# Kernel optimization log

Measured on AMD Instinct MI355X. Metric: run time of the kernel, lower is better.

The kernel has to match this reference:

```python
import jax, jax.numpy as jnp
import numpy as np

N = 100000
NNZ = 3200000
K = 3

def setup_inputs() -> dict:
    key = jax.random.key(0)
    ks = jax.random.split(key, 9)
    return {
        "x": jax.random.normal(ks[0], (N, 128), dtype=jnp.float32),
        "vals": jax.random.uniform(ks[1], (NNZ,), dtype=jnp.float32) * (1.0 / 32.0),
        "W1": jax.random.normal(ks[2], (128 * K, 256), dtype=jnp.float32) * 0.05,
        "b1": jax.random.normal(ks[3], (256,), dtype=jnp.float32) * 0.05,
        "W2": jax.random.normal(ks[4], (256 * K, 64), dtype=jnp.float32) * 0.05,
        "b2": jax.random.normal(ks[5], (64,), dtype=jnp.float32) * 0.05,
        "rows": jax.random.randint(ks[6], (NNZ,), 0, N, dtype=jnp.int32),
        "cols": jax.random.randint(ks[7], (NNZ,), 0, N, dtype=jnp.int32),
        "idx": jax.random.randint(ks[8], (50000,), 0, N, dtype=jnp.int32),
    }

def _spmm(rows, cols, vals, x):
    # sparse [N,N] @ dense [N,F] via gather + segment_sum
    return jax.ops.segment_sum(vals[:, None] * x[cols], rows, num_segments=N)

def _cheb_basis(x, rows, cols, vals, k):
    # Chebyshev recurrence: T0=x, T1=L x, T_m = 2 L T_{m-1} - T_{m-2}
    xs = [x]
    if k > 1:
        x0, x1 = x, _spmm(rows, cols, vals, x)
        xs.append(x1)
        for _ in range(2, k):
            x2 = 2.0 * _spmm(rows, cols, vals, x1) - x0
            xs.append(x2)
            x0, x1 = x1, x2
    # match torch layout: [N, F, K] -> [N, F*K] (per-feature K contiguous)
    return jnp.stack(xs, axis=2).reshape(x.shape[0], -1)

def reference(x, vals, W1, b1, W2, b2, rows, cols, idx):
    h = _cheb_basis(x, rows, cols, vals, K) @ W1 + b1
    h = jax.nn.relu(h)  # dropout omitted (eval mode)
    out = _cheb_basis(h, rows, cols, vals, K) @ W2 + b2
    return out[idx]
```

## Files before the change

kernel.cpp:

```cpp
#include <hip/hip_runtime.h>
#include <hip/hip_bf16.h>

typedef __attribute__((ext_vector_type(8))) __bf16 bf16x8;
typedef __attribute__((ext_vector_type(4))) float floatx4;
typedef unsigned short ushort_t;
typedef unsigned int uint_t;

#define N_NODES 100000
#define NNZ_E   3200000
#define N_IDX   50000
#define NB_BKT  196
#define PTILE   8192
#define PBLOCKS 391

__device__ __forceinline__ float bf2f(uint_t u16) {
  union { float f; uint_t i; } v; v.i = u16 << 16; return v.f;
}
__device__ __forceinline__ unsigned short f2bf(float f) {
  union { float f; uint_t i; } v; v.f = f;
  uint_t x = v.i;
  return (unsigned short)((x + 0x7FFFu + ((x >> 16) & 1u)) >> 16);
}


__global__ __launch_bounds__(256) void k_bhist(const int* __restrict__ rows,
                                               int* __restrict__ bcnt) {
  __shared__ int h[NB_BKT];
  for (int i = threadIdx.x; i < NB_BKT; i += 256) h[i] = 0;
  __syncthreads();
  int base = blockIdx.x * PTILE;
  for (int i = threadIdx.x; i < PTILE; i += 256) {
    int e = base + i;
    if (e < NNZ_E) atomicAdd(&h[rows[e] >> 9], 1);
  }
  __syncthreads();
  for (int i = threadIdx.x; i < NB_BKT; i += 256)
    if (h[i]) atomicAdd(&bcnt[i], h[i]);
}

__global__ void k_bscan(const int* __restrict__ bcnt, int* __restrict__ bbase,
                        int* __restrict__ bcur) {
  __shared__ int ts[256];
  int t = threadIdx.x;
  int v = (t < NB_BKT) ? bcnt[t] : 0;
  ts[t] = v;
  __syncthreads();
  for (int off = 1; off < 256; off <<= 1) {
    int x = ts[t];
    int a = (t >= off) ? ts[t - off] : 0;
    __syncthreads();
    ts[t] = x + a;
    __syncthreads();
  }
  if (t < NB_BKT) {
    int b = (t == 0) ? 0 : ts[t - 1];
    bbase[t] = b;
    bcur[t] = b;
  }
}

__global__ __launch_bounds__(256) void k_part(const int* __restrict__ rows,
                                              const int* __restrict__ cols,
                                              const float* __restrict__ vals,
                                              int* __restrict__ bcur,
                                              int2* __restrict__ tmp) {
  __shared__ int h[NB_BKT];
  for (int i = threadIdx.x; i < NB_BKT; i += 256) h[i] = 0;
  __syncthreads();
  int base = blockIdx.x * PTILE;
  for (int i = threadIdx.x; i < PTILE; i += 256) {
    int e = base + i;
    if (e < NNZ_E) atomicAdd(&h[rows[e] >> 9], 1);
  }
  __syncthreads();
  for (int i = threadIdx.x; i < NB_BKT; i += 256) {
    int c = h[i];
    h[i] = c ? atomicAdd(&bcur[i], c) : 0;
  }
  __syncthreads();
  for (int i = threadIdx.x; i < PTILE; i += 256) {
    int e = base + i;
    if (e < NNZ_E) {
      int rr = rows[e];
      int p = atomicAdd(&h[rr >> 9], 1);
      int2 o;
      o.x = cols[e] | ((rr & 511) << 17);
      o.y = __float_as_int(vals[e]);
      tmp[p] = o;
    }
  }
}

__global__ __launch_bounds__(512) void k_sort(const int* __restrict__ bbase,
                                              const int2* __restrict__ tmp,
                                              int2* __restrict__ edges,
                                              int* __restrict__ rowptr) {
  __shared__ int cnt[512];
  __shared__ int ts[512];
  int b = blockIdx.x, t = threadIdx.x;
  int s = bbase[b];
  int epos = (b == NB_BKT - 1) ? NNZ_E : bbase[b + 1];
  cnt[t] = 0;
  __syncthreads();
  for (int i = s + t; i < epos; i += 512)
    atomicAdd(&cnt[(tmp[i].x >> 17) & 511], 1);
  __syncthreads();
  ts[t] = cnt[t];
  __syncthreads();
  for (int off = 1; off < 512; off <<= 1) {
    int x = ts[t];
    int a = (t >= off) ? ts[t - off] : 0;
    __syncthreads();
    ts[t] = x + a;
    __syncthreads();
  }
  int pre = (t == 0) ? 0 : ts[t - 1];
  int grow = b * 512 + t;
  if (grow < N_NODES) rowptr[grow] = s + pre;
  cnt[t] = s + pre;
  __syncthreads();
  for (int i = s + t; i < epos; i += 512) {
    int2 p = tmp[i];
    int rl = (p.x >> 17) & 511;
    int pos = atomicAdd(&cnt[rl], 1);
    int2 o;
    o.x = p.x & 0x1FFFF;
    o.y = p.y;
    edges[pos] = o;
  }
  if (b == 0 && t == 0) rowptr[N_NODES] = NNZ_E;
}


__global__ void k_cvt(const float4* __restrict__ x, ushort4* __restrict__ xb) {
  int i = blockIdx.x * blockDim.x + threadIdx.x;
  if (i < N_NODES * 128 / 4) {
    float4 v = x[i];
    ushort4 o;
    o.x = f2bf(v.x); o.y = f2bf(v.y); o.z = f2bf(v.z); o.w = f2bf(v.w);
    xb[i] = o;
  }
}


__global__ void k_prepW1(const float* __restrict__ W, ushort_t* __restrict__ Wp) {
  int kp = blockIdx.x;
  int n  = threadIdx.x;
  int ch = kp >> 7;
  int f  = kp & 127;
  float v;
  if (ch == 0)      v = W[(f*3+0)*256+n] - W[(f*3+2)*256+n];
  else if (ch == 1) v = W[(f*3+1)*256+n];
  else              v = 2.0f * W[(f*3+2)*256+n];
  int kb = kp >> 5, kr = kp & 31;
  int lane = ((kr >> 3) << 4) | (n & 15);
  Wp[(((size_t)kb * 16 + (n >> 4)) * 64 + lane) * 8 + (kr & 7)] = f2bf(v);
}

__global__ void k_prepW2(const float* __restrict__ W, ushort_t* __restrict__ Wp) {
  int f = blockIdx.x;
  int c = threadIdx.x;
  int g = c >> 6, n = c & 63;
  float v;
  if (g == 0)      v = W[(f*3+0)*64+n] - W[(f*3+2)*64+n];
  else if (g == 1) v = W[(f*3+1)*64+n];
  else             v = 2.0f * W[(f*3+2)*64+n];
  int kb = f >> 5, kr = f & 31;
  int nb = c >> 4;
  int lane = ((kr >> 3) << 4) | (c & 15);
  Wp[(((size_t)kb * 12 + nb) * 64 + lane) * 8 + (kr & 7)] = f2bf(v);
}


__global__ __launch_bounds__(256) void k_spmm128(
    const int* __restrict__ rowptr, const int2* __restrict__ edges,
    const ushort_t* __restrict__ in, ushort_t* __restrict__ out) {
  int r = blockIdx.x * 4 + (threadIdx.x >> 6);
  int f = threadIdx.x & 63;
  int e0 = rowptr[r], e1 = rowptr[r + 1];
  float a0 = 0.f, a1 = 0.f;
  int e = e0;
  for (; e + 8 <= e1; e += 8) {
    int2 E[8];
#pragma unroll
    for (int j = 0; j < 8; ++j) E[j] = edges[e + j];
    uint_t q[8];
#pragma unroll
    for (int j = 0; j < 8; ++j)
      q[j] = *(const uint_t*)(in + (size_t)E[j].x * 128 + 2 * f);
#pragma unroll
    for (int j = 0; j < 8; ++j) {
      float v = __int_as_float(E[j].y);
      a0 = fmaf(v, bf2f(q[j] & 0xFFFFu), a0);
      a1 = fmaf(v, bf2f(q[j] >> 16), a1);
    }
  }
  for (; e + 4 <= e1; e += 4) {
    int2 E[4];
#pragma unroll
    for (int j = 0; j < 4; ++j) E[j] = edges[e + j];
#pragma unroll
    for (int j = 0; j < 4; ++j) {
      uint_t q = *(const uint_t*)(in + (size_t)E[j].x * 128 + 2 * f);
      float v = __int_as_float(E[j].y);
      a0 = fmaf(v, bf2f(q & 0xFFFFu), a0);
      a1 = fmaf(v, bf2f(q >> 16), a1);
    }
  }
  for (; e < e1; ++e) {
    int2 E = edges[e];
    uint_t q = *(const uint_t*)(in + (size_t)E.x * 128 + 2 * f);
    float v = __int_as_float(E.y);
    a0 = fmaf(v, bf2f(q & 0xFFFFu), a0);
    a1 = fmaf(v, bf2f(q >> 16), a1);
  }
  uint_t o = ((uint_t)f2bf(a1) << 16) | (uint_t)f2bf(a0);
  *(uint_t*)(out + (size_t)r * 128 + 2 * f) = o;
}


__global__ __launch_bounds__(256) void k_spmm64_add(
    const int* __restrict__ rowptr, const int2* __restrict__ edges,
    const ushort_t* __restrict__ p2, const ushort_t* __restrict__ p1,
    ushort_t* __restrict__ u) {
  int r = blockIdx.x * 4 + (threadIdx.x >> 6);
  int lane = threadIdx.x & 63;
  int half = lane >> 5, f = lane & 31;
  int e0 = rowptr[r], e1 = rowptr[r + 1];
  int ne = e1 - e0;
  int hs = (ne + 1) >> 1;
  int e = e0 + half * hs;
  int send = half ? e1 : (e0 + hs);
  float a0 = 0.f, a1 = 0.f;
  for (; e + 4 <= send; e += 4) {
    int2 E[4];
#pragma unroll
    for (int j = 0; j < 4; ++j) E[j] = edges[e + j];
#pragma unroll
    for (int j = 0; j < 4; ++j) {
      uint_t q = *(const uint_t*)(p2 + (size_t)E[j].x * 64 + 2 * f);
      float v = __int_as_float(E[j].y);
      a0 = fmaf(v, bf2f(q & 0xFFFFu), a0);
      a1 = fmaf(v, bf2f(q >> 16), a1);
    }
  }
  for (; e < send; ++e) {
    int2 E = edges[e];
    uint_t q = *(const uint_t*)(p2 + (size_t)E.x * 64 + 2 * f);
    float v = __int_as_float(E.y);
    a0 = fmaf(v, bf2f(q & 0xFFFFu), a0);
    a1 = fmaf(v, bf2f(q >> 16), a1);
  }
  a0 += __shfl_xor(a0, 32);
  a1 += __shfl_xor(a1, 32);
  if (half == 0) {
    uint_t pp = *(const uint_t*)(p1 + (size_t)r * 64 + 2 * f);
    float b0 = a0 + bf2f(pp & 0xFFFFu);
    float b1 = a1 + bf2f(pp >> 16);
    uint_t o = ((uint_t)f2bf(b1) << 16) | (uint_t)f2bf(b0);
    *(uint_t*)(u + (size_t)r * 64 + 2 * f) = o;
  }
}


__global__ __launch_bounds__(256) void k_spmm64_idx(
    const int* __restrict__ rowptr, const int2* __restrict__ edges,
    const ushort_t* __restrict__ u, const float* __restrict__ p0,
    const int* __restrict__ idx, float* __restrict__ out) {
  int o = blockIdx.x * 4 + (threadIdx.x >> 6);
  int r = idx[o];
  int lane = threadIdx.x & 63;
  int half = lane >> 5, f = lane & 31;
  int e0 = rowptr[r], e1 = rowptr[r + 1];
  int ne = e1 - e0;
  int hs = (ne + 1) >> 1;
  int e = e0 + half * hs;
  int send = half ? e1 : (e0 + hs);
  float a0 = 0.f, a1 = 0.f;
  for (; e + 4 <= send; e += 4) {
    int2 E[4];
#pragma unroll
    for (int j = 0; j < 4; ++j) E[j] = edges[e + j];
#pragma unroll
    for (int j = 0; j < 4; ++j) {
      uint_t q = *(const uint_t*)(u + (size_t)E[j].x * 64 + 2 * f);
      float v = __int_as_float(E[j].y);
      a0 = fmaf(v, bf2f(q & 0xFFFFu), a0);
      a1 = fmaf(v, bf2f(q >> 16), a1);
    }
  }
  for (; e < send; ++e) {
    int2 E = edges[e];
    uint_t q = *(const uint_t*)(u + (size_t)E.x * 64 + 2 * f);
    float v = __int_as_float(E.y);
    a0 = fmaf(v, bf2f(q & 0xFFFFu), a0);
    a1 = fmaf(v, bf2f(q >> 16), a1);
  }
  a0 += __shfl_xor(a0, 32);
  a1 += __shfl_xor(a1, 32);
  if (half == 0) {
    float2 b = *(const float2*)(p0 + (size_t)r * 64 + 2 * f);
    float2 w; w.x = b.x + a0; w.y = b.y + a1;
    *(float2*)(out + (size_t)o * 64 + 2 * f) = w;
  }
}


__global__ __launch_bounds__(256) void k_gemm1(
    const ushort_t* __restrict__ A0, const ushort_t* __restrict__ A1,
    const ushort_t* __restrict__ A2, const ushort_t* __restrict__ Bp,
    const float* __restrict__ bias, ushort_t* __restrict__ h) {
  int wid = (blockIdx.x * 256 + threadIdx.x) >> 6;
  int lane = threadIdx.x & 63;
  int mt = wid >> 1, ng = wid & 1;
  int mr = mt * 16 + (lane & 15);
  int ko = (lane >> 4) << 3;
  floatx4 acc[8] = {};
#pragma unroll
  for (int c = 0; c < 3; ++c) {
    const ushort_t* Ab = (c == 0 ? A0 : c == 1 ? A1 : A2) + (size_t)mr * 128 + ko;
#pragma unroll
    for (int kb = 0; kb < 4; ++kb) {
      bf16x8 a = *(const bf16x8*)(Ab + kb * 32);
      int kbg = c * 4 + kb;
      const ushort_t* Bb = Bp + (((size_t)(kbg * 16 + ng * 8)) * 64 + lane) * 8;
#pragma unroll
      for (int nt = 0; nt < 8; ++nt) {
        bf16x8 b = *(const bf16x8*)(Bb + (size_t)nt * 64 * 8);
        acc[nt] = __builtin_amdgcn_mfma_f32_16x16x32_bf16(a, b, acc[nt], 0, 0, 0);
      }
    }
  }
  int col0 = ng * 128 + (lane & 15);
  int r0 = mt * 16 + ((lane >> 4) << 2);
#pragma unroll
  for (int nt = 0; nt < 8; ++nt) {
    int col = col0 + nt * 16;
    float bv = bias[col];
#pragma unroll
    for (int rg = 0; rg < 4; ++rg) {
      float v = acc[nt][rg] + bv;
      v = v > 0.f ? v : 0.f;
      h[(size_t)(r0 + rg) * 256 + col] = f2bf(v);
    }
  }
}


__global__ __launch_bounds__(256) void k_gemm2(
    const ushort_t* __restrict__ A, const ushort_t* __restrict__ Bp,
    const float* __restrict__ bias, float* __restrict__ p0,
    ushort_t* __restrict__ p1, ushort_t* __restrict__ p2) {
  int wid = (blockIdx.x * 256 + threadIdx.x) >> 6;
  if (wid >= 18750) return;
  int lane = threadIdx.x & 63;
  int mt = wid / 3, ng = wid - mt * 3;
  int mr = mt * 16 + (lane & 15);
  int ko = (lane >> 4) << 3;
  floatx4 acc[4] = {};
  const ushort_t* Ab = A + (size_t)mr * 256 + ko;
#pragma unroll
  for (int kb = 0; kb < 8; ++kb) {
    bf16x8 a = *(const bf16x8*)(Ab + kb * 32);
    const ushort_t* Bb = Bp + (((size_t)(kb * 12 + ng * 4)) * 64 + lane) * 8;
#pragma unroll
    for (int nt = 0; nt < 4; ++nt) {
      bf16x8 b = *(const bf16x8*)(Bb + (size_t)nt * 64 * 8);
      acc[nt] = __builtin_amdgcn_mfma_f32_16x16x32_bf16(a, b, acc[nt], 0, 0, 0);
    }
  }
  int c16 = lane & 15;
  int r0 = mt * 16 + ((lane >> 4) << 2);
  if (ng == 0) {
#pragma unroll
    for (int nt = 0; nt < 4; ++nt) {
      float bv = bias[nt * 16 + c16];
#pragma unroll
      for (int rg = 0; rg < 4; ++rg)
        p0[(size_t)(r0 + rg) * 64 + nt * 16 + c16] = acc[nt][rg] + bv;
    }
  } else {
    ushort_t* dst = (ng == 1) ? p1 : p2;
#pragma unroll
    for (int nt = 0; nt < 4; ++nt)
#pragma unroll
      for (int rg = 0; rg < 4; ++rg)
        dst[(size_t)(r0 + rg) * 64 + nt * 16 + c16] = f2bf(acc[nt][rg]);
  }
}


extern "C" void kernel_launch(void* const* d_in, const int* in_sizes, int n_in,
                              void* d_out, int out_size, void* d_ws, size_t ws_size,
                              hipStream_t stream) {
  const float* x    = (const float*)d_in[0];
  const float* vals = (const float*)d_in[1];
  const float* W1   = (const float*)d_in[2];
  const float* b1   = (const float*)d_in[3];
  const float* W2   = (const float*)d_in[4];
  const float* b2   = (const float*)d_in[5];
  const int*   rows = (const int*)d_in[6];
  const int*   cols = (const int*)d_in[7];
  const int*   idx  = (const int*)d_in[8];
  float* out = (float*)d_out;

  char* w = (char*)d_ws;
  size_t off = 0;
  auto take = [&](size_t b) -> char* {
    char* p = w + off;
    off += (b + 255) & ~(size_t)255;
    return p;
  };
  int*      bcnt    = (int*)take((size_t)NB_BKT * 4);
  int*      bbase   = (int*)take((size_t)NB_BKT * 4);
  int*      bcur    = (int*)take((size_t)NB_BKT * 4);
  int*      rowptr  = (int*)take((size_t)(N_NODES + 1) * 4);
  int2*     tmp     = (int2*)take((size_t)NNZ_E * 8);
  int2*     edges   = (int2*)take((size_t)NNZ_E * 8);
  ushort_t* xb      = (ushort_t*)take((size_t)N_NODES * 128 * 2);
  ushort_t* T1a     = (ushort_t*)take((size_t)N_NODES * 128 * 2);
  ushort_t* U1      = (ushort_t*)take((size_t)N_NODES * 128 * 2);
  ushort_t* h       = (ushort_t*)take((size_t)N_NODES * 256 * 2);
  ushort_t* W1p     = (ushort_t*)take((size_t)384 * 256 * 2);
  ushort_t* W2p     = (ushort_t*)take((size_t)256 * 192 * 2);

  float*    p0 = (float*)xb;
  ushort_t* p1 = T1a;
  ushort_t* p2 = T1a + (size_t)N_NODES * 64;
  ushort_t* u  = U1;

  hipMemsetAsync(bcnt, 0, (size_t)NB_BKT * 4, stream);
  k_bhist<<<PBLOCKS, 256, 0, stream>>>(rows, bcnt);
  k_bscan<<<1, 256, 0, stream>>>(bcnt, bbase, bcur);
  k_part<<<PBLOCKS, 256, 0, stream>>>(rows, cols, vals, bcur, tmp);
  k_sort<<<NB_BKT, 512, 0, stream>>>(bbase, tmp, edges, rowptr);

  k_cvt<<<(N_NODES * 128 / 4 + 255) / 256, 256, 0, stream>>>((const float4*)x, (ushort4*)xb);
  k_prepW1<<<384, 256, 0, stream>>>(W1, W1p);
  k_prepW2<<<256, 192, 0, stream>>>(W2, W2p);

  k_spmm128<<<N_NODES / 4, 256, 0, stream>>>(rowptr, edges, xb, T1a);
  k_spmm128<<<N_NODES / 4, 256, 0, stream>>>(rowptr, edges, T1a, U1);
  k_gemm1<<<3125, 256, 0, stream>>>(xb, T1a, U1, W1p, b1, h);

  k_gemm2<<<4688, 256, 0, stream>>>(h, W2p, b2, p0, p1, p2);
  k_spmm64_add<<<N_NODES / 4, 256, 0, stream>>>(rowptr, edges, p2, p1, u);
  k_spmm64_idx<<<N_IDX / 4, 256, 0, stream>>>(rowptr, edges, u, p0, idx, out);
}
```

Baseline: 684.9 us.

## Interleave edges across half-waves with wider gathers and uniform row indices in SpMM

The SpMM kernels now split each row's edges between the two half-waves by interleaving even and odd edges, and reduce the partial sums with a cross-half shuffle. The 128-feature kernel gathers 8 bytes per lane so that each half-wave covers a full row. Row indices are forced into scalar registers with readfirstlane, and a 32-edge unrolled main loop keeps more gathers in flight. This is meant to raise memory-level parallelism and cut per-edge overhead, at the cost of higher register pressure from the 32-entry edge arrays and an extra shuffle reduction.

After: 1.238 ms. 80.8% more time.

```diff
diff --git a/kernel.cpp b/kernel.cpp
--- a/kernel.cpp
+++ b/kernel.cpp
@@ -175,47 +175,80 @@
 __global__ __launch_bounds__(256) void k_spmm128(
     const int* __restrict__ rowptr, const int2* __restrict__ edges,
     const ushort_t* __restrict__ in, ushort_t* __restrict__ out) {
-  int r = blockIdx.x * 4 + (threadIdx.x >> 6);
-  int f = threadIdx.x & 63;
+  int r = __builtin_amdgcn_readfirstlane(blockIdx.x * 4 + (threadIdx.x >> 6));
+  int lane = threadIdx.x & 63;
+  int half = lane >> 5;
+  int l5 = lane & 31;
   int e0 = rowptr[r], e1 = rowptr[r + 1];
-  float a0 = 0.f, a1 = 0.f;
+  float a0 = 0.f, a1 = 0.f, a2 = 0.f, a3 = 0.f;
   int e = e0;
+  for (; e + 32 <= e1; e += 32) {
+    int2 E[32];
+#pragma unroll
+    for (int j = 0; j < 32; ++j) E[j] = edges[e + j];
+    uint2 q[16];
+#pragma unroll
+    for (int j = 0; j < 16; ++j) {
+      int c = half ? E[2*j+1].x : E[2*j].x;
+      q[j] = *(const uint2*)(in + (size_t)c * 128 + 4 * l5);
+    }
+#pragma unroll
+    for (int j = 0; j < 16; ++j) {
+      float v = __int_as_float(half ? E[2*j+1].y : E[2*j].y);
+      a0 = fmaf(v, bf2f(q[j].x & 0xFFFFu), a0);
+      a1 = fmaf(v, bf2f(q[j].x >> 16), a1);
+      a2 = fmaf(v, bf2f(q[j].y & 0xFFFFu), a2);
+      a3 = fmaf(v, bf2f(q[j].y >> 16), a3);
+    }
+  }
   for (; e + 8 <= e1; e += 8) {
     int2 E[8];
 #pragma unroll
     for (int j = 0; j < 8; ++j) E[j] = edges[e + j];
-    uint_t q[8];
-#pragma unroll
-    for (int j = 0; j < 8; ++j)
-      q[j] = *(const uint_t*)(in + (size_t)E[j].x * 128 + 2 * f);
-#pragma unroll
-    for (int j = 0; j < 8; ++j) {
-      float v = __int_as_float(E[j].y);
-      a0 = fmaf(v, bf2f(q[j] & 0xFFFFu), a0);
-      a1 = fmaf(v, bf2f(q[j] >> 16), a1);
-    }
-  }
-  for (; e + 4 <= e1; e += 4) {
-    int2 E[4];
-#pragma unroll
-    for (int j = 0; j < 4; ++j) E[j] = edges[e + j];
+    uint2 q[4];
 #pragma unroll
     for (int j = 0; j < 4; ++j) {
-      uint_t q = *(const uint_t*)(in + (size_t)E[j].x * 128 + 2 * f);
-      float v = __int_as_float(E[j].y);
-      a0 = fmaf(v, bf2f(q & 0xFFFFu), a0);
-      a1 = fmaf(v, bf2f(q >> 16), a1);
-    }
-  }
-  for (; e < e1; ++e) {
+      int c = half ? E[2*j+1].x : E[2*j].x;
+      q[j] = *(const uint2*)(in + (size_t)c * 128 + 4 * l5);
+    }
+#pragma unroll
+    for (int j = 0; j < 4; ++j) {
+      float v = __int_as_float(half ? E[2*j+1].y : E[2*j].y);
+      a0 = fmaf(v, bf2f(q[j].x & 0xFFFFu), a0);
+      a1 = fmaf(v, bf2f(q[j].x >> 16), a1);
+      a2 = fmaf(v, bf2f(q[j].y & 0xFFFFu), a2);
+      a3 = fmaf(v, bf2f(q[j].y >> 16), a3);
+    }
+  }
+  for (; e + 2 <= e1; e += 2) {
+    int2 Ea = edges[e], Eb = edges[e + 1];
+    int c = half ? Eb.x : Ea.x;
+    uint2 q = *(const uint2*)(in + (size_t)c * 128 + 4 * l5);
+    float v = __int_as_float(half ? Eb.y : Ea.y);
+    a0 = fmaf(v, bf2f(q.x & 0xFFFFu), a0);
+    a1 = fmaf(v, bf2f(q.x >> 16), a1);
+    a2 = fmaf(v, bf2f(q.y & 0xFFFFu), a2);
+    a3 = fmaf(v, bf2f(q.y >> 16), a3);
+  }
+  if (e < e1) {
     int2 E = edges[e];
-    uint_t q = *(const uint_t*)(in + (size_t)E.x * 128 + 2 * f);
-    float v = __int_as_float(E.y);
-    a0 = fmaf(v, bf2f(q & 0xFFFFu), a0);
-    a1 = fmaf(v, bf2f(q >> 16), a1);
-  }
-  uint_t o = ((uint_t)f2bf(a1) << 16) | (uint_t)f2bf(a0);
-  *(uint_t*)(out + (size_t)r * 128 + 2 * f) = o;
+    uint2 q = *(const uint2*)(in + (size_t)E.x * 128 + 4 * l5);
+    float v = half ? 0.f : __int_as_float(E.y);
+    a0 = fmaf(v, bf2f(q.x & 0xFFFFu), a0);
+    a1 = fmaf(v, bf2f(q.x >> 16), a1);
+    a2 = fmaf(v, bf2f(q.y & 0xFFFFu), a2);
+    a3 = fmaf(v, bf2f(q.y >> 16), a3);
+  }
+  a0 += __shfl_xor(a0, 32);
+  a1 += __shfl_xor(a1, 32);
+  a2 += __shfl_xor(a2, 32);
+  a3 += __shfl_xor(a3, 32);
+  if (half == 0) {
+    uint2 o2;
+    o2.x = ((uint_t)f2bf(a1) << 16) | (uint_t)f2bf(a0);
+    o2.y = ((uint_t)f2bf(a3) << 16) | (uint_t)f2bf(a2);
+    *(uint2*)(out + (size_t)r * 128 + 4 * l5) = o2;
+  }
 }
 
 
@@ -223,42 +256,70 @@
     const int* __restrict__ rowptr, const int2* __restrict__ edges,
     const ushort_t* __restrict__ p2, const ushort_t* __restrict__ p1,
     ushort_t* __restrict__ u) {
-  int r = blockIdx.x * 4 + (threadIdx.x >> 6);
+  int r = __builtin_amdgcn_readfirstlane(blockIdx.x * 4 + (threadIdx.x >> 6));
   int lane = threadIdx.x & 63;
-  int half = lane >> 5, f = lane & 31;
+  int half = lane >> 5;
+  int l5 = lane & 31;
   int e0 = rowptr[r], e1 = rowptr[r + 1];
-  int ne = e1 - e0;
-  int hs = (ne + 1) >> 1;
-  int e = e0 + half * hs;
-  int send = half ? e1 : (e0 + hs);
   float a0 = 0.f, a1 = 0.f;
-  for (; e + 4 <= send; e += 4) {
-    int2 E[4];
-#pragma unroll
-    for (int j = 0; j < 4; ++j) E[j] = edges[e + j];
+  int e = e0;
+  for (; e + 32 <= e1; e += 32) {
+    int2 E[32];
+#pragma unroll
+    for (int j = 0; j < 32; ++j) E[j] = edges[e + j];
+    uint_t q[16];
+#pragma unroll
+    for (int j = 0; j < 16; ++j) {
+      int c = half ? E[2*j+1].x : E[2*j].x;
+      q[j] = *(const uint_t*)(p2 + (size_t)c * 64 + 2 * l5);
+    }
+#pragma unroll
+    for (int j = 0; j < 16; ++j) {
+      float v = __int_as_float(half ? E[2*j+1].y : E[2*j].y);
+      a0 = fmaf(v, bf2f(q[j] & 0xFFFFu), a0);
+      a1 = fmaf(v, bf2f(q[j] >> 16), a1);
+    }
+  }
+  for (; e + 8 <= e1; e += 8) {
+    int2 E[8];
+#pragma unroll
+    for (int j = 0; j < 8; ++j) E[j] = edges[e + j];
+    uint_t q[4];
 #pragma unroll
     for (int j = 0; j < 4; ++j) {
-      uint_t q = *(const uint_t*)(p2 + (size_t)E[j].x * 64 + 2 * f);
-      float v = __int_as_float(E[j].y);
-      a0 = fmaf(v, bf2f(q & 0xFFFFu), a0);
-      a1 = fmaf(v, bf2f(q >> 16), a1);
-    }
-  }
-  for (; e < send; ++e) {
+      int c = half ? E[2*j+1].x : E[2*j].x;
+      q[j] = *(const uint_t*)(p2 + (size_t)c * 64 + 2 * l5);
+    }
+#pragma unroll
+    for (int j = 0; j < 4; ++j) {
+      float v = __int_as_float(half ? E[2*j+1].y : E[2*j].y);
+      a0 = fmaf(v, bf2f(q[j] & 0xFFFFu), a0);
+      a1 = fmaf(v, bf2f(q[j] >> 16), a1);
+    }
+  }
+  for (; e + 2 <= e1; e += 2) {
+    int2 Ea = edges[e], Eb = edges[e + 1];
+    int c = half ? Eb.x : Ea.x;
+    uint_t q = *(const uint_t*)(p2 + (size_t)c * 64 + 2 * l5);
+    float v = __int_as_float(half ? Eb.y : Ea.y);
+    a0 = fmaf(v, bf2f(q & 0xFFFFu), a0);
+    a1 = fmaf(v, bf2f(q >> 16), a1);
+  }
+  if (e < e1) {
     int2 E = edges[e];
-    uint_t q = *(const uint_t*)(p2 + (size_t)E.x * 64 + 2 * f);
-    float v = __int_as_float(E.y);
+    uint_t q = *(const uint_t*)(p2 + (size_t)E.x * 64 + 2 * l5);
+    float v = half ? 0.f : __int_as_float(E.y);
     a0 = fmaf(v, bf2f(q & 0xFFFFu), a0);
     a1 = fmaf(v, bf2f(q >> 16), a1);
   }
   a0 += __shfl_xor(a0, 32);
   a1 += __shfl_xor(a1, 32);
   if (half == 0) {
-    uint_t pp = *(const uint_t*)(p1 + (size_t)r * 64 + 2 * f);
+    uint_t pp = *(const uint_t*)(p1 + (size_t)r * 64 + 2 * l5);
     float b0 = a0 + bf2f(pp & 0xFFFFu);
     float b1 = a1 + bf2f(pp >> 16);
     uint_t o = ((uint_t)f2bf(b1) << 16) | (uint_t)f2bf(b0);
-    *(uint_t*)(u + (size_t)r * 64 + 2 * f) = o;
+    *(uint_t*)(u + (size_t)r * 64 + 2 * l5) = o;
   }
 }
 
@@ -267,41 +328,69 @@
     const int* __restrict__ rowptr, const int2* __restrict__ edges,
     const ushort_t* __restrict__ u, const float* __restrict__ p0,
     const int* __restrict__ idx, float* __restrict__ out) {
-  int o = blockIdx.x * 4 + (threadIdx.x >> 6);
-  int r = idx[o];
+  int o = __builtin_amdgcn_readfirstlane(blockIdx.x * 4 + (threadIdx.x >> 6));
   int lane = threadIdx.x & 63;
-  int half = lane >> 5, f = lane & 31;
+  int half = lane >> 5;
+  int l5 = lane & 31;
+  int r = __builtin_amdgcn_readfirstlane(idx[o]);
   int e0 = rowptr[r], e1 = rowptr[r + 1];
-  int ne = e1 - e0;
-  int hs = (ne + 1) >> 1;
-  int e = e0 + half * hs;
-  int send = half ? e1 : (e0 + hs);
   float a0 = 0.f, a1 = 0.f;
-  for (; e + 4 <= send; e += 4) {
-    int2 E[4];
-#pragma unroll
-    for (int j = 0; j < 4; ++j) E[j] = edges[e + j];
+  int e = e0;
+  for (; e + 32 <= e1; e += 32) {
+    int2 E[32];
+#pragma unroll
+    for (int j = 0; j < 32; ++j) E[j] = edges[e + j];
+    uint_t q[16];
+#pragma unroll
+    for (int j = 0; j < 16; ++j) {
+      int c = half ? E[2*j+1].x : E[2*j].x;
+      q[j] = *(const uint_t*)(u + (size_t)c * 64 + 2 * l5);
+    }
+#pragma unroll
+    for (int j = 0; j < 16; ++j) {
+      float v = __int_as_float(half ? E[2*j+1].y : E[2*j].y);
+      a0 = fmaf(v, bf2f(q[j] & 0xFFFFu), a0);
+      a1 = fmaf(v, bf2f(q[j] >> 16), a1);
+    }
+  }
+  for (; e + 8 <= e1; e += 8) {
+    int2 E[8];
+#pragma unroll
+    for (int j = 0; j < 8; ++j) E[j] = edges[e + j];
+    uint_t q[4];
 #pragma unroll
     for (int j = 0; j < 4; ++j) {
-      uint_t q = *(const uint_t*)(u + (size_t)E[j].x * 64 + 2 * f);
-      float v = __int_as_float(E[j].y);
-      a0 = fmaf(v, bf2f(q & 0xFFFFu), a0);
-      a1 = fmaf(v, bf2f(q >> 16), a1);
-    }
-  }
-  for (; e < send; ++e) {
+      int c = half ? E[2*j+1].x : E[2*j].x;
+      q[j] = *(const uint_t*)(u + (size_t)c * 64 + 2 * l5);
+    }
+#pragma unroll
+    for (int j = 0; j < 4; ++j) {
+      float v = __int_as_float(half ? E[2*j+1].y : E[2*j].y);
+      a0 = fmaf(v, bf2f(q[j] & 0xFFFFu), a0);
+      a1 = fmaf(v, bf2f(q[j] >> 16), a1);
+    }
+  }
+  for (; e + 2 <= e1; e += 2) {
+    int2 Ea = edges[e], Eb = edges[e + 1];
+    int c = half ? Eb.x : Ea.x;
+    uint_t q = *(const uint_t*)(u + (size_t)c * 64 + 2 * l5);
+    float v = __int_as_float(half ? Eb.y : Ea.y);
+    a0 = fmaf(v, bf2f(q & 0xFFFFu), a0);
+    a1 = fmaf(v, bf2f(q >> 16), a1);
+  }
+  if (e < e1) {
     int2 E = edges[e];
-    uint_t q = *(const uint_t*)(u + (size_t)E.x * 64 + 2 * f);
-    float v = __int_as_float(E.y);
+    uint_t q = *(const uint_t*)(u + (size_t)E.x * 64 + 2 * l5);
+    float v = half ? 0.f : __int_as_float(E.y);
     a0 = fmaf(v, bf2f(q & 0xFFFFu), a0);
     a1 = fmaf(v, bf2f(q >> 16), a1);
   }
   a0 += __shfl_xor(a0, 32);
   a1 += __shfl_xor(a1, 32);
   if (half == 0) {
-    float2 b = *(const float2*)(p0 + (size_t)r * 64 + 2 * f);
+    float2 b = *(const float2*)(p0 + (size_t)r * 64 + 2 * l5);
     float2 w; w.x = b.x + a0; w.y = b.y + a1;
-    *(float2*)(out + (size_t)o * 64 + 2 * f) = w;
+    *(float2*)(out + (size_t)o * 64 + 2 * l5) = w;
   }
 }
 
```
